# Optimization experiments

Hardware: AMD Instinct MI355X
Metric: run time of the kernel (lower is better)

The kernel has to match this reference:

```python
import jax, jax.numpy as jnp
import numpy as np

NUM_HEADS = 12


def setup_inputs() -> dict:
    key = jax.random.key(0)
    k0, k1, k2 = jax.random.split(key, 3)
    B, N, C = 32, 864, 768  # N = 2*t_h*t_w + s_h*s_w = 288 + 576
    x = jax.random.normal(k0, (B, N, C), dtype=jnp.float32)
    W_qkv = jax.random.normal(k1, (C, 3 * C), dtype=jnp.float32) * 0.02
    W_proj = jax.random.normal(k2, (C, C), dtype=jnp.float32) * 0.02
    b_proj = jnp.zeros((C,), dtype=jnp.float32)
    return {"x": x, "W_qkv": W_qkv, "W_proj": W_proj, "b_proj": b_proj,
            "t_h": 12, "t_w": 12, "s_h": 24, "s_w": 24}


def reference(x, W_qkv, W_proj, b_proj, t_h, t_w, s_h, s_w):
    B, N, C = x.shape
    H = NUM_HEADS
    d = C // H
    scale = d ** -0.5
    # qkv projection (no bias), shape [3, B, H, N, d]
    qkv = (x @ W_qkv).reshape(B, N, 3, H, d).transpose(2, 0, 3, 1, 4)
    q, k, v = qkv[0], qkv[1], qkv[2]
    Tt = 2 * t_h * t_w            # temporal (template) query tokens = 288
    Ts = s_h * s_w                # spatial (search) query tokens = 576
    Mt = 2 * ((t_h + 1) // 2) ** 2  # sub-sampled temporal kv tokens = 72
    Ms = (s_h * s_w) // 4           # sub-sampled spatial kv tokens = 144
    q_t, q_s = q[:, :, :Tt], q[:, :, Tt:Tt + Ts]
    k_t, k_s = k[:, :, :Mt], k[:, :, Mt:Mt + Ms]
    v_t, v_s = v[:, :, :Mt], v[:, :, Mt:Mt + Ms]
    # temporal queries attend spatial keys/values
    a_t = jax.nn.softmax(jnp.einsum('bhqd,bhkd->bhqk', q_t, k_s) * scale, axis=-1)
    x_t = jnp.einsum('bhqk,bhkd->bhqd', a_t, v_s).transpose(0, 2, 1, 3).reshape(B, Tt, C)
    # spatial queries attend temporal keys/values
    a_s = jax.nn.softmax(jnp.einsum('bhqd,bhkd->bhqk', q_s, k_t) * scale, axis=-1)
    x_s = jnp.einsum('bhqk,bhkd->bhqd', a_s, v_t).transpose(0, 2, 1, 3).reshape(B, Ts, C)
    out = jnp.concatenate([x_t, x_s], axis=1)  # [B, N, C]
    return out @ W_proj + b_proj
```

## Files before the change

### kernel.cpp

```cpp
#include <hip/hip_runtime.h>
#include <hip/hip_bf16.h>

typedef __attribute__((ext_vector_type(8))) short short8;
typedef __attribute__((ext_vector_type(4))) float floatx4;

#define MFMA16(a, b, c) __builtin_amdgcn_mfma_f32_16x16x32_bf16((a), (b), (c), 0, 0, 0)

static constexpr int Bb = 32, Nn = 864, Cc = 768, Hh = 12;
static constexpr int Mm = Bb * Nn;
static constexpr int KVROWS = 256;

__device__ __forceinline__ void gload_lds16(const __hip_bfloat16* g, __hip_bfloat16* l) {
    __builtin_amdgcn_global_load_lds((const __attribute__((address_space(1))) void*)g,
                                     (__attribute__((address_space(3))) void*)l, 16, 0, 0);
}

static constexpr int CVT_BLKS = (Mm * Cc / 4) / 256;
static constexpr int TQKV_BLKS = (3 * Cc / 32) * (Cc / 32);
static constexpr int TPROJ_BLKS = (Cc / 32) * (Cc / 32);

__global__ __launch_bounds__(256) void prep_kernel(const float* __restrict__ x,
                                                   const float* __restrict__ Wqkv,
                                                   const float* __restrict__ Wproj,
                                                   __hip_bfloat16* __restrict__ xb,
                                                   __hip_bfloat16* __restrict__ WqkvT,
                                                   __hip_bfloat16* __restrict__ WprojT) {
    __shared__ float tile[32][33];
    const int bx = blockIdx.x;
    if (bx < CVT_BLKS) {
        const int i = bx * 256 + threadIdx.x;
        const float4 v = ((const float4*)x)[i];
        __hip_bfloat16 o[4] = {__float2bfloat16(v.x), __float2bfloat16(v.y),
                               __float2bfloat16(v.z), __float2bfloat16(v.w)};
        ((uint2*)xb)[i] = *(const uint2*)o;
        return;
    }
    const float* in;
    __hip_bfloat16* out;
    int R, C, bid;
    if (bx < CVT_BLKS + TQKV_BLKS) {
        bid = bx - CVT_BLKS; in = Wqkv; out = WqkvT; R = Cc; C = 3 * Cc;
    } else {
        bid = bx - CVT_BLKS - TQKV_BLKS; in = Wproj; out = WprojT; R = Cc; C = Cc;
    }
    const int c0 = (bid % (C / 32)) * 32, r0 = (bid / (C / 32)) * 32;
    const int tx = threadIdx.x & 31, ty = threadIdx.x >> 5;
#pragma unroll
    for (int i = 0; i < 32; i += 8)
        tile[ty + i][tx] = in[(size_t)(r0 + ty + i) * C + c0 + tx];
    __syncthreads();
#pragma unroll
    for (int i = 0; i < 32; i += 8)
        out[(size_t)(c0 + ty + i) * R + r0 + tx] = __float2bfloat16(tile[tx][ty + i]);
}

static constexpr int QBLKS = 6 * (Mm / 128);
static constexpr int KVBLKS = 12 * (Bb * KVROWS / 128);
static constexpr int QKV_NWG = QBLKS + KVBLKS;

__global__ __launch_bounds__(256, 5) void gemm_qkv(const __hip_bfloat16* __restrict__ A,
                                                   const __hip_bfloat16* __restrict__ WqkvT,
                                                   __hip_bfloat16* __restrict__ Qbuf,
                                                   __hip_bfloat16* __restrict__ Kbuf,
                                                   __hip_bfloat16* __restrict__ VTbuf) {
    __shared__ __align__(16) char SMEM[32768];
    __hip_bfloat16* As = (__hip_bfloat16*)SMEM;
    __hip_bfloat16* Bs = As + 8192;

    const int braw = (int)blockIdx.x;
    const int sid = (braw & 7) * (QKV_NWG / 8) + (braw >> 3);

    int arow0, orow0, btrow, ncol0, bb = 0, keybase = 0;
    __hip_bfloat16* Out;
    int Nout;
    bool vmode = false;
    if (sid < QBLKS) {
        const int nt = sid % 6, mt = sid / 6;
        arow0 = mt * 128; orow0 = arow0;
        btrow = nt * 128; ncol0 = nt * 128;
        Out = Qbuf; Nout = Cc;
    } else {
        const int s = sid - QBLKS;
        const int nt = s % 12, mt = s / 12;
        bb = mt >> 1; keybase = (mt & 1) << 7;
        arow0 = bb * Nn + keybase;
        btrow = Cc + nt * 128;
        if (nt < 6) {
            orow0 = bb * KVROWS + keybase; ncol0 = nt * 128;
            Out = Kbuf; Nout = Cc;
        } else {
            vmode = true; ncol0 = (nt - 6) * 128;
            Out = nullptr; Nout = 0; orow0 = 0;
        }
    }

    const int t = threadIdx.x;
    const int lane = t & 63, wave = t >> 6;
    const int wm = (wave >> 1) * 64, wn = (wave & 1) * 64;
    const int ln = lane & 15, quad = lane >> 4;

    floatx4 acc[4][4] = {};

    const int r0 = t >> 2;
    const int cst = (t & 3) * 8;
    const __hip_bfloat16* Ag = A + (size_t)(arow0 + r0) * Cc + cst;
    const __hip_bfloat16* Bg = WqkvT + (size_t)(btrow + r0) * Cc + cst;
    const size_t rowskip = (size_t)64 * Cc;

    for (int k0 = 0; k0 < Cc; k0 += 64) {
        gload_lds16(Ag + k0,                &As[t * 8]);
        gload_lds16(Ag + k0 + rowskip,      &As[2048 + t * 8]);
        gload_lds16(Ag + k0 + 32,           &As[4096 + t * 8]);
        gload_lds16(Ag + k0 + 32 + rowskip, &As[6144 + t * 8]);
        gload_lds16(Bg + k0,                &Bs[t * 8]);
        gload_lds16(Bg + k0 + rowskip,      &Bs[2048 + t * 8]);
        gload_lds16(Bg + k0 + 32,           &Bs[4096 + t * 8]);
        gload_lds16(Bg + k0 + 32 + rowskip, &Bs[6144 + t * 8]);
        __syncthreads();

#pragma unroll
        for (int s = 0; s < 2; s++) {
            short8 af[4], bfr[4];
#pragma unroll
            for (int i = 0; i < 4; i++)
                af[i] = *(const short8*)&As[s * 4096 + (wm + i * 16 + ln) * 32 + quad * 8];
#pragma unroll
            for (int j = 0; j < 4; j++)
                bfr[j] = *(const short8*)&Bs[s * 4096 + (wn + j * 16 + ln) * 32 + quad * 8];
#pragma unroll
            for (int i = 0; i < 4; i++)
#pragma unroll
                for (int j = 0; j < 4; j++)
                    acc[i][j] = MFMA16(af[i], bfr[j], acc[i][j]);
        }
        __syncthreads();
    }

    if (!vmode) {
#pragma unroll
        for (int j = 0; j < 4; j++) {
            const int n = ncol0 + wn + j * 16 + ln;
#pragma unroll
            for (int i = 0; i < 4; i++) {
                const int mrow = orow0 + wm + i * 16 + quad * 4;
#pragma unroll
                for (int r = 0; r < 4; r++)
                    Out[(size_t)(mrow + r) * Nout + n] = __float2bfloat16(acc[i][j][r]);
            }
        }
        return;
    }

    __hip_bfloat16* T = (__hip_bfloat16*)SMEM;
#pragma unroll
    for (int pass = 0; pass < 2; pass++) {
        if ((wave & 1) == pass) {
#pragma unroll
            for (int j = 0; j < 4; j++) {
                const int ddl = j * 16 + ln;
#pragma unroll
                for (int i = 0; i < 4; i++) {
                    const int key = wm + i * 16 + quad * 4;
                    const __hip_bfloat162 lo =
                        __float22bfloat162_rn(make_float2(acc[i][j][0], acc[i][j][1]));
                    const __hip_bfloat162 hi =
                        __float22bfloat162_rn(make_float2(acc[i][j][2], acc[i][j][3]));
                    uint2 pk = make_uint2(*(const unsigned int*)&lo,
                                          *(const unsigned int*)&hi);
                    *(uint2*)&T[ddl * 136 + key] = pk;
                }
            }
        }
        __syncthreads();
#pragma unroll
        for (int it = 0; it < 4; it++) {
            const int ldd = it * 16 + (t >> 4);
            const int kk = (t & 15) * 8;
            const short8 v = *(const short8*)&T[ldd * 136 + kk];
            *(short8*)&VTbuf[(size_t)(bb * Cc + ncol0 + pass * 64 + ldd) * KVROWS +
                             keybase + kk] = v;
        }
        if (pass == 0) __syncthreads();
    }
}

__global__ __launch_bounds__(256) void gemm_proj(const __hip_bfloat16* __restrict__ A,
                                                 const __hip_bfloat16* __restrict__ BT,
                                                 float* __restrict__ Cout,
                                                 const float* __restrict__ bias) {
    __shared__ __align__(16) __hip_bfloat16 As[8192];
    __shared__ __align__(16) __hip_bfloat16 Bs[8192];
    const int gx = (int)gridDim.x;
    const int nwg = gx * (int)gridDim.y;
    const int braw = (int)blockIdx.y * gx + (int)blockIdx.x;
    const int sid = (braw & 7) * (nwg >> 3) + (braw >> 3);
    const int mt = sid / gx, nt = sid - mt * gx;
    const int m0 = mt << 7, n0 = nt * 128;
    const int t = threadIdx.x;
    const int lane = t & 63, wave = t >> 6;
    const int wm = (wave >> 1) * 64, wn = (wave & 1) * 64;
    const int ln = lane & 15, quad = lane >> 4;

    floatx4 acc[4][4] = {};
    const int r0 = t >> 2, cst = (t & 3) * 8;
    const __hip_bfloat16* Ag = A + (size_t)(m0 + r0) * Cc + cst;
    const __hip_bfloat16* Bg = BT + (size_t)(n0 + r0) * Cc + cst;
    const size_t rowskip = (size_t)64 * Cc;

    for (int k0 = 0; k0 < Cc; k0 += 64) {
        gload_lds16(Ag + k0,                &As[t * 8]);
        gload_lds16(Ag + k0 + rowskip,      &As[2048 + t * 8]);
        gload_lds16(Ag + k0 + 32,           &As[4096 + t * 8]);
        gload_lds16(Ag + k0 + 32 + rowskip, &As[6144 + t * 8]);
        gload_lds16(Bg + k0,                &Bs[t * 8]);
        gload_lds16(Bg + k0 + rowskip,      &Bs[2048 + t * 8]);
        gload_lds16(Bg + k0 + 32,           &Bs[4096 + t * 8]);
        gload_lds16(Bg + k0 + 32 + rowskip, &Bs[6144 + t * 8]);
        __syncthreads();
#pragma unroll
        for (int s = 0; s < 2; s++) {
            short8 af[4], bfr[4];
#pragma unroll
            for (int i = 0; i < 4; i++)
                af[i] = *(const short8*)&As[s * 4096 + (wm + i * 16 + ln) * 32 + quad * 8];
#pragma unroll
            for (int j = 0; j < 4; j++)
                bfr[j] = *(const short8*)&Bs[s * 4096 + (wn + j * 16 + ln) * 32 + quad * 8];
#pragma unroll
            for (int i = 0; i < 4; i++)
#pragma unroll
                for (int j = 0; j < 4; j++)
                    acc[i][j] = MFMA16(af[i], bfr[j], acc[i][j]);
        }
        __syncthreads();
    }
#pragma unroll
    for (int j = 0; j < 4; j++) {
        const int n = n0 + wn + j * 16 + ln;
        const float bv = bias[n];
#pragma unroll
        for (int i = 0; i < 4; i++) {
            const int mrow = m0 + wm + i * 16 + quad * 4;
#pragma unroll
            for (int r = 0; r < 4; r++)
                Cout[(size_t)(mrow + r) * Cc + n] = acc[i][j][r] + bv;
        }
    }
}

template <int L, int QOFF, int KVOFF, int NQT, int NCH>
__device__ __forceinline__ void attn_part(const __hip_bfloat16* __restrict__ qb,
                                          const __hip_bfloat16* __restrict__ kb,
                                          const __hip_bfloat16* __restrict__ vtb,
                                          __hip_bfloat16* __restrict__ attn,
                                          int qc, int h, int b,
                                          __hip_bfloat16* VTs) {
    constexpr int KPAD = NCH * 32;
    constexpr int NB8 = KPAD / 8;
    constexpr int VSTR = KPAD + 8;
    const int t = threadIdx.x, lane = t & 63;
    const int ln = lane & 15, quad = lane >> 4;

    const __hip_bfloat16* kbase = kb + (size_t)(b * KVROWS + KVOFF) * Cc + h * 64;
    const __hip_bfloat16* vtbase =
        vtb + (size_t)(b * Cc + h * 64) * KVROWS + KVOFF;

    for (int c = t; c < 64 * NB8; c += 256) {
        const int dd = c / NB8, kbk = c - dd * NB8;
        const int colp8 = (kbk + dd) % NB8;
        uint4 val = make_uint4(0u, 0u, 0u, 0u);
        if (kbk * 8 < L)
            val = *(const uint4*)(vtbase + (size_t)dd * KVROWS + kbk * 8);
        *(uint4*)&VTs[dd * VSTR + colp8 * 8] = val;
    }
    __syncthreads();

    const int qt = qc * 4 + (t >> 6);
    if (qt >= NQT) return;

    const __hip_bfloat16* qrow = qb + (size_t)(b * Nn + QOFF + qt * 16 + ln) * Cc + h * 64;
    const short8 aq0 = *(const short8*)(qrow + quad * 8);
    const short8 aq1 = *(const short8*)(qrow + 32 + quad * 8);

    int ddm[4];
#pragma unroll
    for (int j = 0; j < 4; j++) ddm[j] = (j * 16 + ln) % NB8;

    float dsum = 0.0f;
    floatx4 acco[4] = {};
    constexpr float CSC = 0.18033688011112042f;

#pragma unroll
    for (int ch = 0; ch < NCH; ch++) {
        unsigned int pk[2][2];
#pragma unroll
        for (int ti2 = 0; ti2 < 2; ti2++) {
            const int ti = ch * 2 + ti2;
            if (ti * 16 >= L) {
                pk[ti2][0] = 0u; pk[ti2][1] = 0u;
                continue;
            }
            const __hip_bfloat16* krow = kbase + (size_t)(ti * 16 + ln) * Cc;
            const short8 k0 = *(const short8*)(krow + quad * 8);
            const short8 k1 = *(const short8*)(krow + 32 + quad * 8);
            floatx4 s = {0.f, 0.f, 0.f, 0.f};
            s = MFMA16(k0, aq0, s);
            s = MFMA16(k1, aq1, s);
            float p[4];
#pragma unroll
            for (int r = 0; r < 4; r++) {
                float e = exp2f(s[r] * CSC);
                if (ti * 16 + 16 > L)
                    if (ti * 16 + quad * 4 + r >= L) e = 0.0f;
                p[r] = e;
                dsum += e;
            }
            const __hip_bfloat162 lo = __float22bfloat162_rn(make_float2(p[0], p[1]));
            const __hip_bfloat162 hi = __float22bfloat162_rn(make_float2(p[2], p[3]));
            pk[ti2][0] = *(const unsigned int*)&lo;
            pk[ti2][1] = *(const unsigned int*)&hi;
        }
        const int srcA = ln + ((quad & 1) << 5);
        const int srcB = srcA + 16;
        const unsigned int c0 = (unsigned int)__shfl((int)pk[0][0], srcA);
        const unsigned int c1 = (unsigned int)__shfl((int)pk[0][1], srcA);
        const unsigned int c2 = (unsigned int)__shfl((int)pk[0][0], srcB);
        const unsigned int c3 = (unsigned int)__shfl((int)pk[0][1], srcB);
        const unsigned int d0 = (unsigned int)__shfl((int)pk[1][0], srcA);
        const unsigned int d1 = (unsigned int)__shfl((int)pk[1][1], srcA);
        const unsigned int d2 = (unsigned int)__shfl((int)pk[1][0], srcB);
        const unsigned int d3 = (unsigned int)__shfl((int)pk[1][1], srcB);
        const bool hi2 = quad >= 2;
        union { unsigned int u[4]; short8 v; } pf;
        pf.u[0] = hi2 ? d0 : c0;
        pf.u[1] = hi2 ? d1 : c1;
        pf.u[2] = hi2 ? d2 : c2;
        pf.u[3] = hi2 ? d3 : c3;
#pragma unroll
        for (int j = 0; j < 4; j++) {
            int cb = ch * 4 + quad + ddm[j];
            if (cb >= NB8) cb -= NB8;
            const short8 vt = *(const short8*)&VTs[(j * 16 + ln) * VSTR + cb * 8];
            acco[j] = MFMA16(vt, pf.v, acco[j]);
        }
    }

    dsum += __shfl_xor(dsum, 16);
    dsum += __shfl_xor(dsum, 32);
    const float inv = 1.0f / dsum;

    const size_t orow = (size_t)(b * Nn + QOFF + qt * 16 + ln) * Cc + h * 64;
#pragma unroll
    for (int j = 0; j < 4; j++) {
        const __hip_bfloat162 lo =
            __float22bfloat162_rn(make_float2(acco[j][0] * inv, acco[j][1] * inv));
        const __hip_bfloat162 hi =
            __float22bfloat162_rn(make_float2(acco[j][2] * inv, acco[j][3] * inv));
        uint2 o = make_uint2(*(const unsigned int*)&lo, *(const unsigned int*)&hi);
        *(uint2*)&attn[orow + j * 16 + quad * 4] = o;
    }
}

__global__ __launch_bounds__(256, 5) void attn_fused(const __hip_bfloat16* __restrict__ qb,
                                                     const __hip_bfloat16* __restrict__ kb,
                                                     const __hip_bfloat16* __restrict__ vtb,
                                                     __hip_bfloat16* __restrict__ attn) {
    __shared__ __align__(16) __hip_bfloat16 VTs[64 * 168];
    constexpr int NB = 14 * 12 * 32;
    const int rid = (int)blockIdx.x + 14 * ((int)blockIdx.y + 12 * (int)blockIdx.z);
    const int vid = (rid & 7) * (NB / 8) + (rid >> 3);
    const int qc = vid % 14, g = vid / 14;
    const int h = g % 12, bq = g / 12;
    if (qc < 5)
        attn_part<144, 0, 72, 18, 5>(qb, kb, vtb, attn, qc, h, bq, VTs);
    else
        attn_part<72, 288, 0, 36, 3>(qb, kb, vtb, attn, qc - 5, h, bq, VTs);
}

extern "C" void kernel_launch(void* const* d_in, const int* in_sizes, int n_in,
                              void* d_out, int out_size, void* d_ws, size_t ws_size,
                              hipStream_t stream) {
    const float* x     = (const float*)d_in[0];
    const float* Wqkv  = (const float*)d_in[1];
    const float* Wproj = (const float*)d_in[2];
    const float* bproj = (const float*)d_in[3];
    float* out = (float*)d_out;

    char* ws = (char*)d_ws;
    __hip_bfloat16* xb     = (__hip_bfloat16*)ws;
    __hip_bfloat16* WqkvT  = (__hip_bfloat16*)(ws + 42467328);
    __hip_bfloat16* WprojT = (__hip_bfloat16*)(ws + 46006272);
    __hip_bfloat16* Qbuf   = (__hip_bfloat16*)(ws + 47185920);
    __hip_bfloat16* Kbuf   = (__hip_bfloat16*)(ws + 89653248);
    __hip_bfloat16* VTbuf  = (__hip_bfloat16*)(ws + 102236160);
    __hip_bfloat16* attn   = (__hip_bfloat16*)ws;

    prep_kernel<<<CVT_BLKS + TQKV_BLKS + TPROJ_BLKS, 256, 0, stream>>>(x, Wqkv, Wproj, xb,
                                                                       WqkvT, WprojT);
    gemm_qkv<<<QKV_NWG, 256, 0, stream>>>(xb, WqkvT, Qbuf, Kbuf, VTbuf);
    attn_fused<<<dim3(14, Hh, Bb), 256, 0, stream>>>(Qbuf, Kbuf, VTbuf, attn);
    gemm_proj<<<dim3(Cc / 128, Mm / 128), 256, 0, stream>>>(attn, WprojT, out, bproj);
}
```

Baseline: 360.4 us.

## Store K and V row-major in one buffer, transpose V in attention LDS

The QKV GEMM epilogue no longer transposes V through shared memory. It writes K and V together as a row-major [rows, 2C] buffer. The attention kernel now loads V rows and scatters them, transposed, into its LDS tile element by element using a rotated column index. This moves the transpose cost from the GEMM epilogue into the attention staging. The trade is scalar 2-byte LDS writes and the loss of the launch-bounds occupancy hint on the GEMM.

```diff
diff --git a/kernel.cpp b/kernel.cpp
--- a/kernel.cpp
+++ b/kernel.cpp
@@ -8,6 +8,7 @@
 
 static constexpr int Bb = 32, Nn = 864, Cc = 768, Hh = 12;
 static constexpr int Mm = Bb * Nn;
+static constexpr int NKV = 2 * Cc;
 static constexpr int KVROWS = 256;
 
 __device__ __forceinline__ void gload_lds16(const __hip_bfloat16* g, __hip_bfloat16* l) {
@@ -58,40 +59,32 @@
 static constexpr int KVBLKS = 12 * (Bb * KVROWS / 128);
 static constexpr int QKV_NWG = QBLKS + KVBLKS;
 
-__global__ __launch_bounds__(256, 5) void gemm_qkv(const __hip_bfloat16* __restrict__ A,
-                                                   const __hip_bfloat16* __restrict__ WqkvT,
-                                                   __hip_bfloat16* __restrict__ Qbuf,
-                                                   __hip_bfloat16* __restrict__ Kbuf,
-                                                   __hip_bfloat16* __restrict__ VTbuf) {
-    __shared__ __align__(16) char SMEM[32768];
-    __hip_bfloat16* As = (__hip_bfloat16*)SMEM;
-    __hip_bfloat16* Bs = As + 8192;
+__global__ __launch_bounds__(256) void gemm_qkv2(const __hip_bfloat16* __restrict__ A,
+                                                 const __hip_bfloat16* __restrict__ WqkvT,
+                                                 __hip_bfloat16* __restrict__ Qbuf,
+                                                 __hip_bfloat16* __restrict__ KVbuf) {
+    __shared__ __align__(16) __hip_bfloat16 As[8192];
+    __shared__ __align__(16) __hip_bfloat16 Bs[8192];
 
     const int braw = (int)blockIdx.x;
     const int sid = (braw & 7) * (QKV_NWG / 8) + (braw >> 3);
 
-    int arow0, orow0, btrow, ncol0, bb = 0, keybase = 0;
+    int arow0, orow0, btrow0, ncol0, Nout;
     __hip_bfloat16* Out;
-    int Nout;
-    bool vmode = false;
     if (sid < QBLKS) {
         const int nt = sid % 6, mt = sid / 6;
         arow0 = mt * 128; orow0 = arow0;
-        btrow = nt * 128; ncol0 = nt * 128;
+        btrow0 = nt * 128; ncol0 = nt * 128;
         Out = Qbuf; Nout = Cc;
     } else {
         const int s = sid - QBLKS;
         const int nt = s % 12, mt = s / 12;
-        bb = mt >> 1; keybase = (mt & 1) << 7;
+        const int bb = mt >> 1, keybase = (mt & 1) << 7;
         arow0 = bb * Nn + keybase;
-        btrow = Cc + nt * 128;
-        if (nt < 6) {
-            orow0 = bb * KVROWS + keybase; ncol0 = nt * 128;
-            Out = Kbuf; Nout = Cc;
-        } else {
-            vmode = true; ncol0 = (nt - 6) * 128;
-            Out = nullptr; Nout = 0; orow0 = 0;
-        }
+        orow0 = bb * KVROWS + keybase;
+        btrow0 = Cc + nt * 128;
+        ncol0 = nt * 128;
+        Out = KVbuf; Nout = NKV;
     }
 
     const int t = threadIdx.x;
@@ -104,7 +97,7 @@
     const int r0 = t >> 2;
     const int cst = (t & 3) * 8;
     const __hip_bfloat16* Ag = A + (size_t)(arow0 + r0) * Cc + cst;
-    const __hip_bfloat16* Bg = WqkvT + (size_t)(btrow + r0) * Cc + cst;
+    const __hip_bfloat16* Bg = WqkvT + (size_t)(btrow0 + r0) * Cc + cst;
     const size_t rowskip = (size_t)64 * Cc;
 
     for (int k0 = 0; k0 < Cc; k0 += 64) {
@@ -136,51 +129,16 @@
         __syncthreads();
     }
 
-    if (!vmode) {
-#pragma unroll
-        for (int j = 0; j < 4; j++) {
-            const int n = ncol0 + wn + j * 16 + ln;
-#pragma unroll
-            for (int i = 0; i < 4; i++) {
-                const int mrow = orow0 + wm + i * 16 + quad * 4;
-#pragma unroll
-                for (int r = 0; r < 4; r++)
-                    Out[(size_t)(mrow + r) * Nout + n] = __float2bfloat16(acc[i][j][r]);
-            }
-        }
-        return;
-    }
-
-    __hip_bfloat16* T = (__hip_bfloat16*)SMEM;
-#pragma unroll
-    for (int pass = 0; pass < 2; pass++) {
-        if ((wave & 1) == pass) {
-#pragma unroll
-            for (int j = 0; j < 4; j++) {
-                const int ddl = j * 16 + ln;
-#pragma unroll
-                for (int i = 0; i < 4; i++) {
-                    const int key = wm + i * 16 + quad * 4;
-                    const __hip_bfloat162 lo =
-                        __float22bfloat162_rn(make_float2(acc[i][j][0], acc[i][j][1]));
-                    const __hip_bfloat162 hi =
-                        __float22bfloat162_rn(make_float2(acc[i][j][2], acc[i][j][3]));
-                    uint2 pk = make_uint2(*(const unsigned int*)&lo,
-                                          *(const unsigned int*)&hi);
-                    *(uint2*)&T[ddl * 136 + key] = pk;
-                }
-            }
-        }
-        __syncthreads();
-#pragma unroll
-        for (int it = 0; it < 4; it++) {
-            const int ldd = it * 16 + (t >> 4);
-            const int kk = (t & 15) * 8;
-            const short8 v = *(const short8*)&T[ldd * 136 + kk];
-            *(short8*)&VTbuf[(size_t)(bb * Cc + ncol0 + pass * 64 + ldd) * KVROWS +
-                             keybase + kk] = v;
-        }
-        if (pass == 0) __syncthreads();
+#pragma unroll
+    for (int j = 0; j < 4; j++) {
+        const int n = ncol0 + wn + j * 16 + ln;
+#pragma unroll
+        for (int i = 0; i < 4; i++) {
+            const int mrow = orow0 + wm + i * 16 + quad * 4;
+#pragma unroll
+            for (int r = 0; r < 4; r++)
+                Out[(size_t)(mrow + r) * Nout + n] = __float2bfloat16(acc[i][j][r]);
+        }
     }
 }
 
@@ -250,41 +208,40 @@
 
 template <int L, int QOFF, int KVOFF, int NQT, int NCH>
 __device__ __forceinline__ void attn_part(const __hip_bfloat16* __restrict__ qb,
-                                          const __hip_bfloat16* __restrict__ kb,
-                                          const __hip_bfloat16* __restrict__ vtb,
+                                          const __hip_bfloat16* __restrict__ kv,
                                           __hip_bfloat16* __restrict__ attn,
                                           int qc, int h, int b,
                                           __hip_bfloat16* VTs) {
     constexpr int KPAD = NCH * 32;
-    constexpr int NB8 = KPAD / 8;
     constexpr int VSTR = KPAD + 8;
-    const int t = threadIdx.x, lane = t & 63;
+    const int t = threadIdx.x, lane = t & 63, wave = t >> 6;
     const int ln = lane & 15, quad = lane >> 4;
-
-    const __hip_bfloat16* kbase = kb + (size_t)(b * KVROWS + KVOFF) * Cc + h * 64;
-    const __hip_bfloat16* vtbase =
-        vtb + (size_t)(b * Cc + h * 64) * KVROWS + KVOFF;
-
-    for (int c = t; c < 64 * NB8; c += 256) {
-        const int dd = c / NB8, kbk = c - dd * NB8;
-        const int colp8 = (kbk + dd) % NB8;
-        uint4 val = make_uint4(0u, 0u, 0u, 0u);
-        if (kbk * 8 < L)
-            val = *(const uint4*)(vtbase + (size_t)dd * KVROWS + kbk * 8);
-        *(uint4*)&VTs[dd * VSTR + colp8 * 8] = val;
+    const __hip_bfloat16 z16 = __float2bfloat16(0.0f);
+
+    const __hip_bfloat16* kbase = kv + (size_t)(b * KVROWS + KVOFF) * NKV + h * 64;
+    const __hip_bfloat16* vbase = kbase + Cc;
+
+    for (int c = t; c < KPAD * 8; c += 256) {
+        const int key = c >> 3, s8 = c & 7, d0 = s8 * 8;
+        const int colp = (key + 8 * s8) % KPAD;
+        if (key < L) {
+            uint4 raw = *(const uint4*)(vbase + (size_t)key * NKV + d0);
+            const __hip_bfloat16* pv = (const __hip_bfloat16*)&raw;
+#pragma unroll
+            for (int jj = 0; jj < 8; jj++) VTs[(d0 + jj) * VSTR + colp] = pv[jj];
+        } else {
+#pragma unroll
+            for (int jj = 0; jj < 8; jj++) VTs[(d0 + jj) * VSTR + colp] = z16;
+        }
     }
     __syncthreads();
 
-    const int qt = qc * 4 + (t >> 6);
+    const int qt = qc * 4 + wave;
     if (qt >= NQT) return;
 
     const __hip_bfloat16* qrow = qb + (size_t)(b * Nn + QOFF + qt * 16 + ln) * Cc + h * 64;
     const short8 aq0 = *(const short8*)(qrow + quad * 8);
     const short8 aq1 = *(const short8*)(qrow + 32 + quad * 8);
-
-    int ddm[4];
-#pragma unroll
-    for (int j = 0; j < 4; j++) ddm[j] = (j * 16 + ln) % NB8;
 
     float dsum = 0.0f;
     floatx4 acco[4] = {};
@@ -300,7 +257,7 @@
                 pk[ti2][0] = 0u; pk[ti2][1] = 0u;
                 continue;
             }
-            const __hip_bfloat16* krow = kbase + (size_t)(ti * 16 + ln) * Cc;
+            const __hip_bfloat16* krow = kbase + (size_t)(ti * 16 + ln) * NKV;
             const short8 k0 = *(const short8*)(krow + quad * 8);
             const short8 k1 = *(const short8*)(krow + 32 + quad * 8);
             floatx4 s = {0.f, 0.f, 0.f, 0.f};
@@ -338,9 +295,9 @@
         pf.u[3] = hi2 ? d3 : c3;
 #pragma unroll
         for (int j = 0; j < 4; j++) {
-            int cb = ch * 4 + quad + ddm[j];
-            if (cb >= NB8) cb -= NB8;
-            const short8 vt = *(const short8*)&VTs[(j * 16 + ln) * VSTR + cb * 8];
+            const int dd = j * 16 + ln;
+            const int colp = (ch * 32 + quad * 8 + ((dd >> 3) << 3)) % KPAD;
+            const short8 vt = *(const short8*)&VTs[dd * VSTR + colp];
             acco[j] = MFMA16(vt, pf.v, acco[j]);
         }
     }
@@ -362,8 +319,7 @@
 }
 
 __global__ __launch_bounds__(256, 5) void attn_fused(const __hip_bfloat16* __restrict__ qb,
-                                                     const __hip_bfloat16* __restrict__ kb,
-                                                     const __hip_bfloat16* __restrict__ vtb,
+                                                     const __hip_bfloat16* __restrict__ kv,
                                                      __hip_bfloat16* __restrict__ attn) {
     __shared__ __align__(16) __hip_bfloat16 VTs[64 * 168];
     constexpr int NB = 14 * 12 * 32;
@@ -372,9 +328,9 @@
     const int qc = vid % 14, g = vid / 14;
     const int h = g % 12, bq = g / 12;
     if (qc < 5)
-        attn_part<144, 0, 72, 18, 5>(qb, kb, vtb, attn, qc, h, bq, VTs);
+        attn_part<144, 0, 72, 18, 5>(qb, kv, attn, qc, h, bq, VTs);
     else
-        attn_part<72, 288, 0, 36, 3>(qb, kb, vtb, attn, qc - 5, h, bq, VTs);
+        attn_part<72, 288, 0, 36, 3>(qb, kv, attn, qc - 5, h, bq, VTs);
 }
 
 extern "C" void kernel_launch(void* const* d_in, const int* in_sizes, int n_in,
@@ -391,13 +347,12 @@
     __hip_bfloat16* WqkvT  = (__hip_bfloat16*)(ws + 42467328);
     __hip_bfloat16* WprojT = (__hip_bfloat16*)(ws + 46006272);
     __hip_bfloat16* Qbuf   = (__hip_bfloat16*)(ws + 47185920);
-    __hip_bfloat16* Kbuf   = (__hip_bfloat16*)(ws + 89653248);
-    __hip_bfloat16* VTbuf  = (__hip_bfloat16*)(ws + 102236160);
+    __hip_bfloat16* KVbuf  = (__hip_bfloat16*)(ws + 89653248);
     __hip_bfloat16* attn   = (__hip_bfloat16*)ws;
 
     prep_kernel<<<CVT_BLKS + TQKV_BLKS + TPROJ_BLKS, 256, 0, stream>>>(x, Wqkv, Wproj, xb,
                                                                        WqkvT, WprojT);
-    gemm_qkv<<<QKV_NWG, 256, 0, stream>>>(xb, WqkvT, Qbuf, Kbuf, VTbuf);
-    attn_fused<<<dim3(14, Hh, Bb), 256, 0, stream>>>(Qbuf, Kbuf, VTbuf, attn);
+    gemm_qkv2<<<QKV_NWG, 256, 0, stream>>>(xb, WqkvT, Qbuf, KVbuf);
+    attn_fused<<<dim3(14, Hh, Bb), 256, 0, stream>>>(Qbuf, KVbuf, attn);
     gemm_proj<<<dim3(Cc / 128, Mm / 128), 256, 0, stream>>>(attn, WprojT, out, bproj);
 }
```

Measured after the change: 341.2 us. 5.3% less time.
